# Kernel optimization log

Measured on AMD Instinct MI355X. Metric: run time of the kernel, lower is better.

## Reference

```python
import jax, jax.numpy as jnp
import numpy as np

NEG_INF = -9.0e15  # matches torch's -9000000000000000.0 mask value
ALPHA = 0.2        # LeakyReLU negative slope from init_kwargs


def setup_inputs() -> dict:
    key = jax.random.key(0)
    k1, k2, k3, k4, k5 = jax.random.split(key, 5)
    B, N, D, A = 64, 128, 128, 1000
    hidden = jax.random.normal(k1, (B, N, D), dtype=jnp.float32)
    adj = jax.random.randint(k2, (B, N, N), 0, 5)  # edge types 0..4 (0 = masked)
    a = jax.random.normal(k3, (D, 4), dtype=jnp.float32) * 0.1  # stacked a_0..a_3
    A_attr_sess = jax.random.uniform(k4, (B, N, A), dtype=jnp.float32)
    attr_embedding = jax.random.normal(k5, (A, D), dtype=jnp.float32)
    return {"hidden": hidden, "adj": adj, "a": a,
            "A_attr_sess": A_attr_sess, "attr_embedding": attr_embedding}


def reference(hidden, adj, a, A_attr_sess, attr_embedding):
    # a_input[b,i,j,:] = leaky_relu(h[b,i,:] * h[b,j,:])  -> [B,N,N,D]
    a_input = jax.nn.leaky_relu(hidden[:, :, None, :] * hidden[:, None, :, :],
                                negative_slope=ALPHA)
    # four edge-type scores in one contraction: [B,N,N,4]
    e = jnp.einsum('bijd,dk->bijk', a_input, a)
    # masked selection by adjacency edge type (later writes override earlier)
    alpha = jnp.full(adj.shape, NEG_INF, dtype=e.dtype)
    alpha = jnp.where(adj == 1, e[..., 0], alpha)
    alpha = jnp.where(adj == 2, e[..., 1], alpha)
    alpha = jnp.where(adj == 3, e[..., 2], alpha)
    alpha = jnp.where(adj == 4, e[..., 3], alpha)
    attn = jax.nn.softmax(alpha, axis=-1)        # [B,N,N]
    output = jnp.einsum('bij,bjd->bid', attn, hidden)  # [B,N,D]
    attr_sess = jnp.einsum('bna,ad->bnd', A_attr_sess, attr_embedding)
    return output, attr_sess
```

## Files before the change

### kernel.cpp

```cpp
#include <hip/hip_runtime.h>

#define BB 64
#define NN 128
#define DD 128
#define AA 1000
#define KPAD 1024
#define NEG_INF (-9.0e15f)

typedef __attribute__((ext_vector_type(8))) short short8;
typedef __attribute__((ext_vector_type(4))) float floatx4;
typedef __attribute__((ext_vector_type(4))) unsigned int uintx4;
typedef __attribute__((ext_vector_type(2))) unsigned int uintx2;

__device__ __forceinline__ float bflo(unsigned int u) { return __uint_as_float(u << 16); }
__device__ __forceinline__ float bfhi(unsigned int u) { return __uint_as_float(u & 0xffff0000u); }
__device__ __forceinline__ unsigned int packbf(float f0, float f1) {
  return (__float_as_uint(f0) >> 16) | (__float_as_uint(f1) & 0xffff0000u);
}
__device__ __forceinline__ unsigned short bf_rne(float f) {
  unsigned int u = __float_as_uint(f);
  return (unsigned short)((u + 0x7fffu + ((u >> 16) & 1u)) >> 16);
}
__device__ __forceinline__ unsigned int packbf_rne(float f0, float f1) {
  return (unsigned int)bf_rne(f0) | ((unsigned int)bf_rne(f1) << 16);
}
__device__ __forceinline__ short8 u2s(uintx4 v) {
  union { uintx4 u; short8 s; } x; x.u = v; return x.s;
}

__global__ __launch_bounds__(256) void prep_kernel(
    const float* __restrict__ hidden, const float* __restrict__ emb,
    unsigned short* __restrict__ ET, unsigned short* __restrict__ HTg)
{
  const int t = threadIdx.x;
  const int bid = blockIdx.x;
  if (bid < BB) {
    __shared__ float hsf[NN * 129];
    const float* hb = hidden + (size_t)bid * NN * DD;
    #pragma unroll
    for (int u = 0; u < 16; ++u) {
      int e = u * 1024 + t * 4;
      float4 v = *reinterpret_cast<const float4*>(hb + e);
      int r = e >> 7, c = e & 127;
      float* d = &hsf[r * 129 + c];
      d[0] = v.x; d[1] = v.y; d[2] = v.z; d[3] = v.w;
    }
    __syncthreads();
    unsigned short* ht16 = HTg + (size_t)bid * NN * DD;
    #pragma unroll
    for (int u = 0; u < 8; ++u) {
      int e = u * 2048 + t * 8;
      int dI = e >> 7, il = e & 127;
      float x[8];
      #pragma unroll
      for (int j = 0; j < 8; ++j) x[j] = hsf[(il + j) * 129 + dI];
      uintx4 o;
      o.x = packbf_rne(x[0], x[1]); o.y = packbf_rne(x[2], x[3]);
      o.z = packbf_rne(x[4], x[5]); o.w = packbf_rne(x[6], x[7]);
      *reinterpret_cast<uintx4*>(ht16 + e) = o;
    }
  } else {
    int c = bid - BB;
    int k0 = t * 4;
    float x[4];
    #pragma unroll
    for (int j = 0; j < 4; ++j) {
      int k = k0 + j;
      x[j] = (k < AA) ? emb[(size_t)k * DD + c] : 0.f;
    }
    uintx2 o;
    o.x = packbf_rne(x[0], x[1]);
    o.y = packbf_rne(x[2], x[3]);
    *reinterpret_cast<uintx2*>(ET + (size_t)c * KPAD + k0) = o;
  }
}

struct AttnSmem {
  __align__(16) unsigned short Hs[NN * 128];
  union {
    __align__(16) unsigned short As[4 * 16 * 256];
    struct {
      __align__(16) float Sa[16 * 129];
      __align__(16) unsigned short W[16 * 128];
    } sw;
  } u2;
  __align__(16) float saf[4 * 256];
};

#define BK 64
struct AttrSmem {
  __align__(16) unsigned short ETs[2][DD * BK];
  __align__(16) unsigned short As2[2][32 * BK];
};

union FusedSmem { AttnSmem a; AttrSmem g; };

__device__ __forceinline__ void attn_body(
    AttnSmem& s, const float* __restrict__ hidden,
    const int* __restrict__ adj, const float* __restrict__ amat,
    const unsigned short* __restrict__ HTg, float* __restrict__ out0)
{
  const int t = threadIdx.x;
  const int L = t & 63, w = t >> 6;
  const int lr = L & 15, lq = L >> 4;
  const int b = blockIdx.x >> 3;
  const int i0 = (blockIdx.x & 7) * 16;

  const int* adjb = adj + ((size_t)b * NN + i0) * NN;
  int adjv[8];
  #pragma unroll
  for (int nt = 0; nt < 2; ++nt)
    #pragma unroll
    for (int r = 0; r < 4; ++r)
      adjv[nt * 4 + r] = adjb[(lq * 4 + r) * NN + w * 32 + nt * 16 + lr];

  const float* hb = hidden + (size_t)b * NN * DD;
  #pragma unroll
  for (int u = 0; u < 8; ++u) {
    int id = u * 256 + t;
    int r = id >> 4, c = id & 15;
    const float* src = hb + r * 128 + c * 8;
    float4 v0 = *reinterpret_cast<const float4*>(src);
    float4 v1 = *reinterpret_cast<const float4*>(src + 4);
    uintx4 o;
    o.x = packbf_rne(v0.x, v0.y); o.y = packbf_rne(v0.z, v0.w);
    o.z = packbf_rne(v1.x, v1.y); o.w = packbf_rne(v1.z, v1.w);
    *reinterpret_cast<uintx4*>(&s.Hs[r * 128 + ((c ^ (r & 15)) << 3)]) = o;
  }
  {
    float v1 = amat[t], v2 = amat[t + 256];
    int dI = t >> 2, k = t & 3;
    s.saf[k * 256 + dI] = 0.6f * v1;
    s.saf[k * 256 + 128 + dI] = 0.4f * v1;
    s.saf[k * 256 + 64 + dI] = 0.6f * v2;
    s.saf[k * 256 + 192 + dI] = 0.4f * v2;
  }
  __syncthreads();

  #pragma unroll
  for (int u = 0; u < 8; ++u) {
    int id = u * 256 + t;
    int k = id >> 9, ii = (id >> 5) & 15, c = id & 31;
    int srow = i0 + ii;
    int dchunk = c & 15;
    uintx4 hv = *reinterpret_cast<const uintx4*>(
        &s.Hs[srow * 128 + ((dchunk ^ (srow & 15)) << 3)]);
    if (c & 16) {
      hv.x &= 0x7fff7fffu; hv.y &= 0x7fff7fffu;
      hv.z &= 0x7fff7fffu; hv.w &= 0x7fff7fffu;
    }
    const float* sf = &s.saf[k * 256 + c * 8];
    uintx4 o;
    o.x = packbf(bflo(hv.x) * sf[0], bfhi(hv.x) * sf[1]);
    o.y = packbf(bflo(hv.y) * sf[2], bfhi(hv.y) * sf[3]);
    o.z = packbf(bflo(hv.z) * sf[4], bfhi(hv.z) * sf[5]);
    o.w = packbf(bflo(hv.w) * sf[6], bfhi(hv.w) * sf[7]);
    *reinterpret_cast<uintx4*>(&s.u2.As[k * 4096 + ii * 256 + ((c ^ ii) << 3)]) = o;
  }
  __syncthreads();

  floatx4 acc[4][2];
  #pragma unroll
  for (int k = 0; k < 4; ++k)
    #pragma unroll
    for (int nt = 0; nt < 2; ++nt) acc[k][nt] = floatx4{0.f, 0.f, 0.f, 0.f};

  #pragma unroll
  for (int kt = 0; kt < 8; ++kt) {
    int ca = lq + 4 * kt;
    short8 afr[4];
    #pragma unroll
    for (int k = 0; k < 4; ++k)
      afr[k] = *reinterpret_cast<const short8*>(
          &s.u2.As[k * 4096 + lr * 256 + ((ca ^ lr) << 3)]);
    int cb = lq + 4 * (kt & 3);
    short8 bfr[2];
    #pragma unroll
    for (int nt = 0; nt < 2; ++nt) {
      int jrow = w * 32 + nt * 16 + lr;
      uintx4 hv = *reinterpret_cast<const uintx4*>(
          &s.Hs[jrow * 128 + ((cb ^ (jrow & 15)) << 3)]);
      if (kt >= 4) {
        hv.x &= 0x7fff7fffu; hv.y &= 0x7fff7fffu;
        hv.z &= 0x7fff7fffu; hv.w &= 0x7fff7fffu;
      }
      bfr[nt] = u2s(hv);
    }
    #pragma unroll
    for (int k = 0; k < 4; ++k)
      #pragma unroll
      for (int nt = 0; nt < 2; ++nt)
        acc[k][nt] = __builtin_amdgcn_mfma_f32_16x16x32_bf16(
            afr[k], bfr[nt], acc[k][nt], 0, 0, 0);
  }
  __syncthreads();

  short8 pvb[2][4];
  const unsigned short* ht = HTg + (size_t)b * NN * DD;
  #pragma unroll
  for (int nt = 0; nt < 2; ++nt)
    #pragma unroll
    for (int kt = 0; kt < 4; ++kt) {
      int dI = w * 32 + nt * 16 + lr;
      pvb[nt][kt] = *reinterpret_cast<const short8*>(ht + dI * 128 + kt * 32 + lq * 8);
    }

  #pragma unroll
  for (int nt = 0; nt < 2; ++nt)
    #pragma unroll
    for (int r = 0; r < 4; ++r) {
      int ii = lq * 4 + r;
      int j = w * 32 + nt * 16 + lr;
      int ad = adjv[nt * 4 + r];
      float al = NEG_INF;
      al = (ad == 1) ? acc[0][nt][r] : al;
      al = (ad == 2) ? acc[1][nt][r] : al;
      al = (ad == 3) ? acc[2][nt][r] : al;
      al = (ad == 4) ? acc[3][nt][r] : al;
      s.u2.sw.Sa[ii * 129 + j] = al;
    }
  __syncthreads();

  #pragma unroll
  for (int p = 0; p < 4; ++p) {
    int ii = w * 4 + p;
    float a1 = s.u2.sw.Sa[ii * 129 + L];
    float a2 = s.u2.sw.Sa[ii * 129 + 64 + L];
    float m = fmaxf(a1, a2);
    #pragma unroll
    for (int off = 32; off > 0; off >>= 1) m = fmaxf(m, __shfl_xor(m, off, 64));
    float e1 = __expf(fmaxf(a1 - m, -80.f));
    float e2 = __expf(fmaxf(a2 - m, -80.f));
    float ss = e1 + e2;
    #pragma unroll
    for (int off = 32; off > 0; off >>= 1) ss += __shfl_xor(ss, off, 64);
    float inv = 1.f / ss;
    int j2 = L + 64;
    s.u2.sw.W[ii * 128 + (((L >> 3) ^ ii) << 3) + (L & 7)] = bf_rne(e1 * inv);
    s.u2.sw.W[ii * 128 + (((j2 >> 3) ^ ii) << 3) + (j2 & 7)] = bf_rne(e2 * inv);
  }
  __syncthreads();

  floatx4 oacc[2];
  oacc[0] = floatx4{0.f, 0.f, 0.f, 0.f};
  oacc[1] = floatx4{0.f, 0.f, 0.f, 0.f};
  #pragma unroll
  for (int kt = 0; kt < 4; ++kt) {
    int c = lq + 4 * kt;
    short8 wf = *reinterpret_cast<const short8*>(
        &s.u2.sw.W[lr * 128 + ((c ^ lr) << 3)]);
    #pragma unroll
    for (int nt = 0; nt < 2; ++nt)
      oacc[nt] = __builtin_amdgcn_mfma_f32_16x16x32_bf16(
          wf, pvb[nt][kt], oacc[nt], 0, 0, 0);
  }
  float* ob = out0 + ((size_t)b * NN + i0) * DD;
  #pragma unroll
  for (int nt = 0; nt < 2; ++nt)
    #pragma unroll
    for (int r = 0; r < 4; ++r)
      ob[(lq * 4 + r) * DD + w * 32 + nt * 16 + lr] = oacc[nt][r];
}

__device__ __forceinline__ void attr_body(
    AttrSmem& s, const float* __restrict__ Aattr,
    const unsigned short* __restrict__ ET, float* __restrict__ out1)
{
  const int t = threadIdx.x;
  const int L = t & 63, w = t >> 6;
  const int lr = L & 15, lq = L >> 4;
  const int r0 = (blockIdx.x - 512) * 32;

  float4 pa0, pa1;
  uintx4 pe[4];
  const int ar = t >> 3, ak = (t & 7) * 8;
  const int ec = t >> 1, ej0 = (t & 1) * 4;

  auto fetch = [&](int it) {
    int kb = it * BK;
    int k4 = kb + ak;
    float4 z = {0.f, 0.f, 0.f, 0.f};
    pa0 = (k4 < AA) ? *reinterpret_cast<const float4*>(Aattr + (size_t)(r0 + ar) * AA + k4) : z;
    pa1 = (k4 + 4 < AA) ? *reinterpret_cast<const float4*>(Aattr + (size_t)(r0 + ar) * AA + k4 + 4) : z;
    #pragma unroll
    for (int q = 0; q < 4; ++q)
      pe[q] = *reinterpret_cast<const uintx4*>(ET + (size_t)ec * KPAD + kb + (ej0 + q) * 8);
  };
  auto stage = [&](int buf) {
    uintx4 o;
    o.x = packbf(pa0.x, pa0.y); o.y = packbf(pa0.z, pa0.w);
    o.z = packbf(pa1.x, pa1.y); o.w = packbf(pa1.z, pa1.w);
    int ac = t & 7;
    *reinterpret_cast<uintx4*>(&s.As2[buf][ar * BK + ((ac ^ (ar & 7)) << 3)]) = o;
    #pragma unroll
    for (int q = 0; q < 4; ++q)
      *reinterpret_cast<uintx4*>(&s.ETs[buf][ec * BK + (((ej0 + q) ^ (ec & 7)) << 3)]) = pe[q];
  };

  floatx4 acc[2][2];
  #pragma unroll
  for (int mt = 0; mt < 2; ++mt)
    #pragma unroll
    for (int nt = 0; nt < 2; ++nt) acc[mt][nt] = floatx4{0.f, 0.f, 0.f, 0.f};

  fetch(0);
  for (int it = 0; it < 16; ++it) {
    stage(it & 1);
    __syncthreads();
    if (it < 15) fetch(it + 1);
    #pragma unroll
    for (int ks = 0; ks < 2; ++ks) {
      int c = lq + 4 * ks;
      short8 af[2], bf[2];
      #pragma unroll
      for (int mt = 0; mt < 2; ++mt) {
        int row = mt * 16 + lr;
        af[mt] = *reinterpret_cast<const short8*>(
            &s.As2[it & 1][row * BK + ((c ^ (row & 7)) << 3)]);
      }
      #pragma unroll
      for (int nt = 0; nt < 2; ++nt) {
        int n = w * 32 + nt * 16 + lr;
        bf[nt] = *reinterpret_cast<const short8*>(
            &s.ETs[it & 1][n * BK + ((c ^ (n & 7)) << 3)]);
      }
      #pragma unroll
      for (int mt = 0; mt < 2; ++mt)
        #pragma unroll
        for (int nt = 0; nt < 2; ++nt)
          acc[mt][nt] = __builtin_amdgcn_mfma_f32_16x16x32_bf16(
              af[mt], bf[nt], acc[mt][nt], 0, 0, 0);
    }
  }

  float* ob = out1 + (size_t)r0 * DD;
  #pragma unroll
  for (int mt = 0; mt < 2; ++mt)
    #pragma unroll
    for (int nt = 0; nt < 2; ++nt)
      #pragma unroll
      for (int r = 0; r < 4; ++r)
        ob[(mt * 16 + lq * 4 + r) * DD + w * 32 + nt * 16 + lr] = acc[mt][nt][r];
}

__global__ __launch_bounds__(256, 3) void fused_kernel(
    const float* __restrict__ hidden, const int* __restrict__ adj,
    const float* __restrict__ amat, const float* __restrict__ Aattr,
    const unsigned short* __restrict__ ET, const unsigned short* __restrict__ HTg,
    float* __restrict__ out0, float* __restrict__ out1)
{
  __shared__ FusedSmem sm;
  if (blockIdx.x < 512) attn_body(sm.a, hidden, adj, amat, HTg, out0);
  else                  attr_body(sm.g, Aattr, ET, out1);
}

extern "C" void kernel_launch(void* const* d_in, const int* in_sizes, int n_in,
                              void* d_out, int out_size, void* d_ws, size_t ws_size,
                              hipStream_t stream) {
  const float* hidden = (const float*)d_in[0];
  const int*   adj    = (const int*)d_in[1];
  const float* amat   = (const float*)d_in[2];
  const float* Aattr  = (const float*)d_in[3];
  const float* emb    = (const float*)d_in[4];

  float* out0 = (float*)d_out;
  float* out1 = out0 + (size_t)BB * NN * DD;

  unsigned short* ET  = (unsigned short*)d_ws;
  unsigned short* HTg = ET + (size_t)DD * KPAD;

  prep_kernel<<<BB + DD, 256, 0, stream>>>(hidden, emb, ET, HTg);
  fused_kernel<<<768, 256, 0, stream>>>(hidden, adj, amat, Aattr, ET, HTg,
                                        out0, out1);
}
```

Measured before the change: 106.8 us.

## Fold prep kernel into fused kernel and compute A-fragments on the fly

Removes the separate prep kernel. Embedding transposition and bf16 conversion now happen inside the attribute GEMM staging, and the P·V operand is read transposed straight from the shared hidden tile instead of a global HT buffer. The attention A-operand is built in registers per k-step instead of being staged in shared memory. Softmax is done in MFMA register layout with cross-wave reductions through small shared arrays. Block roles are interleaved 2:1 and occupancy is raised to 4 blocks per SM. These changes remove a launch and global round-trips, in exchange for extra per-thread ALU work and scalar 16-bit LDS gathers.

```diff
diff --git a/kernel.cpp b/kernel.cpp
--- a/kernel.cpp
+++ b/kernel.cpp
@@ -4,13 +4,11 @@
 #define NN 128
 #define DD 128
 #define AA 1000
-#define KPAD 1024
 #define NEG_INF (-9.0e15f)
 
 typedef __attribute__((ext_vector_type(8))) short short8;
 typedef __attribute__((ext_vector_type(4))) float floatx4;
 typedef __attribute__((ext_vector_type(4))) unsigned int uintx4;
-typedef __attribute__((ext_vector_type(2))) unsigned int uintx2;
 
 __device__ __forceinline__ float bflo(unsigned int u) { return __uint_as_float(u << 16); }
 __device__ __forceinline__ float bfhi(unsigned int u) { return __uint_as_float(u & 0xffff0000u); }
@@ -28,69 +26,17 @@
   union { uintx4 u; short8 s; } x; x.u = v; return x.s;
 }
 
-__global__ __launch_bounds__(256) void prep_kernel(
-    const float* __restrict__ hidden, const float* __restrict__ emb,
-    unsigned short* __restrict__ ET, unsigned short* __restrict__ HTg)
-{
-  const int t = threadIdx.x;
-  const int bid = blockIdx.x;
-  if (bid < BB) {
-    __shared__ float hsf[NN * 129];
-    const float* hb = hidden + (size_t)bid * NN * DD;
-    #pragma unroll
-    for (int u = 0; u < 16; ++u) {
-      int e = u * 1024 + t * 4;
-      float4 v = *reinterpret_cast<const float4*>(hb + e);
-      int r = e >> 7, c = e & 127;
-      float* d = &hsf[r * 129 + c];
-      d[0] = v.x; d[1] = v.y; d[2] = v.z; d[3] = v.w;
-    }
-    __syncthreads();
-    unsigned short* ht16 = HTg + (size_t)bid * NN * DD;
-    #pragma unroll
-    for (int u = 0; u < 8; ++u) {
-      int e = u * 2048 + t * 8;
-      int dI = e >> 7, il = e & 127;
-      float x[8];
-      #pragma unroll
-      for (int j = 0; j < 8; ++j) x[j] = hsf[(il + j) * 129 + dI];
-      uintx4 o;
-      o.x = packbf_rne(x[0], x[1]); o.y = packbf_rne(x[2], x[3]);
-      o.z = packbf_rne(x[4], x[5]); o.w = packbf_rne(x[6], x[7]);
-      *reinterpret_cast<uintx4*>(ht16 + e) = o;
-    }
-  } else {
-    int c = bid - BB;
-    int k0 = t * 4;
-    float x[4];
-    #pragma unroll
-    for (int j = 0; j < 4; ++j) {
-      int k = k0 + j;
-      x[j] = (k < AA) ? emb[(size_t)k * DD + c] : 0.f;
-    }
-    uintx2 o;
-    o.x = packbf_rne(x[0], x[1]);
-    o.y = packbf_rne(x[2], x[3]);
-    *reinterpret_cast<uintx2*>(ET + (size_t)c * KPAD + k0) = o;
-  }
-}
-
 struct AttnSmem {
   __align__(16) unsigned short Hs[NN * 128];
-  union {
-    __align__(16) unsigned short As[4 * 16 * 256];
-    struct {
-      __align__(16) float Sa[16 * 129];
-      __align__(16) unsigned short W[16 * 128];
-    } sw;
-  } u2;
-  __align__(16) float saf[4 * 256];
+  __align__(16) unsigned short W[16 * 128];
+  __align__(16) unsigned short safb[4 * 256];
+  float wredM[4 * 16];
+  float wredS[4 * 16];
 };
 
-#define BK 64
 struct AttrSmem {
-  __align__(16) unsigned short ETs[2][DD * BK];
-  __align__(16) unsigned short As2[2][32 * BK];
+  __align__(16) unsigned short ETs[2][DD * 64];
+  __align__(16) unsigned short As2[2][32 * 64];
 };
 
 union FusedSmem { AttnSmem a; AttrSmem g; };
@@ -98,13 +44,13 @@
 __device__ __forceinline__ void attn_body(
     AttnSmem& s, const float* __restrict__ hidden,
     const int* __restrict__ adj, const float* __restrict__ amat,
-    const unsigned short* __restrict__ HTg, float* __restrict__ out0)
+    float* __restrict__ out0, int aid)
 {
   const int t = threadIdx.x;
   const int L = t & 63, w = t >> 6;
   const int lr = L & 15, lq = L >> 4;
-  const int b = blockIdx.x >> 3;
-  const int i0 = (blockIdx.x & 7) * 16;
+  const int b = aid >> 3;
+  const int i0 = (aid & 7) * 16;
 
   const int* adjb = adj + ((size_t)b * NN + i0) * NN;
   int adjv[8];
@@ -130,35 +76,13 @@
   {
     float v1 = amat[t], v2 = amat[t + 256];
     int dI = t >> 2, k = t & 3;
-    s.saf[k * 256 + dI] = 0.6f * v1;
-    s.saf[k * 256 + 128 + dI] = 0.4f * v1;
-    s.saf[k * 256 + 64 + dI] = 0.6f * v2;
-    s.saf[k * 256 + 192 + dI] = 0.4f * v2;
+    s.safb[k * 256 + dI]        = bf_rne(0.6f * v1);
+    s.safb[k * 256 + 128 + dI]  = bf_rne(0.4f * v1);
+    s.safb[k * 256 + 64 + dI]   = bf_rne(0.6f * v2);
+    s.safb[k * 256 + 192 + dI]  = bf_rne(0.4f * v2);
   }
   __syncthreads();
 
-  #pragma unroll
-  for (int u = 0; u < 8; ++u) {
-    int id = u * 256 + t;
-    int k = id >> 9, ii = (id >> 5) & 15, c = id & 31;
-    int srow = i0 + ii;
-    int dchunk = c & 15;
-    uintx4 hv = *reinterpret_cast<const uintx4*>(
-        &s.Hs[srow * 128 + ((dchunk ^ (srow & 15)) << 3)]);
-    if (c & 16) {
-      hv.x &= 0x7fff7fffu; hv.y &= 0x7fff7fffu;
-      hv.z &= 0x7fff7fffu; hv.w &= 0x7fff7fffu;
-    }
-    const float* sf = &s.saf[k * 256 + c * 8];
-    uintx4 o;
-    o.x = packbf(bflo(hv.x) * sf[0], bfhi(hv.x) * sf[1]);
-    o.y = packbf(bflo(hv.y) * sf[2], bfhi(hv.y) * sf[3]);
-    o.z = packbf(bflo(hv.z) * sf[4], bfhi(hv.z) * sf[5]);
-    o.w = packbf(bflo(hv.w) * sf[6], bfhi(hv.w) * sf[7]);
-    *reinterpret_cast<uintx4*>(&s.u2.As[k * 4096 + ii * 256 + ((c ^ ii) << 3)]) = o;
-  }
-  __syncthreads();
-
   floatx4 acc[4][2];
   #pragma unroll
   for (int k = 0; k < 4; ++k)
@@ -167,13 +91,27 @@
 
   #pragma unroll
   for (int kt = 0; kt < 8; ++kt) {
-    int ca = lq + 4 * kt;
+    const int cb = lq + 4 * (kt & 3);
+    const int aoff = (kt >= 4) ? 128 : 0;
+    uintx4 ha = *reinterpret_cast<const uintx4*>(
+        &s.Hs[(i0 + lr) * 128 + ((cb ^ lr) << 3)]);
+    if (kt >= 4) {
+      ha.x &= 0x7fff7fffu; ha.y &= 0x7fff7fffu;
+      ha.z &= 0x7fff7fffu; ha.w &= 0x7fff7fffu;
+    }
+    const float h0 = bflo(ha.x), h1 = bfhi(ha.x), h2 = bflo(ha.y), h3 = bfhi(ha.y);
+    const float h4 = bflo(ha.z), h5 = bfhi(ha.z), h6 = bflo(ha.w), h7 = bfhi(ha.w);
     short8 afr[4];
     #pragma unroll
-    for (int k = 0; k < 4; ++k)
-      afr[k] = *reinterpret_cast<const short8*>(
-          &s.u2.As[k * 4096 + lr * 256 + ((ca ^ lr) << 3)]);
-    int cb = lq + 4 * (kt & 3);
+    for (int k = 0; k < 4; ++k) {
+      uintx4 sv = *reinterpret_cast<const uintx4*>(&s.safb[k * 256 + aoff + cb * 8]);
+      uintx4 o;
+      o.x = packbf(h0 * bflo(sv.x), h1 * bfhi(sv.x));
+      o.y = packbf(h2 * bflo(sv.y), h3 * bfhi(sv.y));
+      o.z = packbf(h4 * bflo(sv.z), h5 * bfhi(sv.z));
+      o.w = packbf(h6 * bflo(sv.w), h7 * bfhi(sv.w));
+      afr[k] = u2s(o);
+    }
     short8 bfr[2];
     #pragma unroll
     for (int nt = 0; nt < 2; ++nt) {
@@ -193,52 +131,61 @@
         acc[k][nt] = __builtin_amdgcn_mfma_f32_16x16x32_bf16(
             afr[k], bfr[nt], acc[k][nt], 0, 0, 0);
   }
+
+  float al[2][4];
+  #pragma unroll
+  for (int nt = 0; nt < 2; ++nt)
+    #pragma unroll
+    for (int r = 0; r < 4; ++r) {
+      int ad = adjv[nt * 4 + r];
+      float v = NEG_INF;
+      v = (ad == 1) ? acc[0][nt][r] : v;
+      v = (ad == 2) ? acc[1][nt][r] : v;
+      v = (ad == 3) ? acc[2][nt][r] : v;
+      v = (ad == 4) ? acc[3][nt][r] : v;
+      al[nt][r] = v;
+    }
+
+  float mr[4];
+  #pragma unroll
+  for (int r = 0; r < 4; ++r) mr[r] = fmaxf(al[0][r], al[1][r]);
+  #pragma unroll
+  for (int off = 1; off < 16; off <<= 1)
+    #pragma unroll
+    for (int r = 0; r < 4; ++r) mr[r] = fmaxf(mr[r], __shfl_xor(mr[r], off, 64));
+  if (lr == 0)
+    #pragma unroll
+    for (int r = 0; r < 4; ++r) s.wredM[w * 16 + lq * 4 + r] = mr[r];
   __syncthreads();
 
-  short8 pvb[2][4];
-  const unsigned short* ht = HTg + (size_t)b * NN * DD;
+  float ex[2][4], sr[4];
+  #pragma unroll
+  for (int r = 0; r < 4; ++r) {
+    int i = lq * 4 + r;
+    float m = fmaxf(fmaxf(s.wredM[i], s.wredM[16 + i]),
+                    fmaxf(s.wredM[32 + i], s.wredM[48 + i]));
+    ex[0][r] = __expf(fmaxf(al[0][r] - m, -80.f));
+    ex[1][r] = __expf(fmaxf(al[1][r] - m, -80.f));
+    sr[r] = ex[0][r] + ex[1][r];
+  }
+  #pragma unroll
+  for (int off = 1; off < 16; off <<= 1)
+    #pragma unroll
+    for (int r = 0; r < 4; ++r) sr[r] += __shfl_xor(sr[r], off, 64);
+  if (lr == 0)
+    #pragma unroll
+    for (int r = 0; r < 4; ++r) s.wredS[w * 16 + lq * 4 + r] = sr[r];
+  __syncthreads();
+
   #pragma unroll
   for (int nt = 0; nt < 2; ++nt)
     #pragma unroll
-    for (int kt = 0; kt < 4; ++kt) {
-      int dI = w * 32 + nt * 16 + lr;
-      pvb[nt][kt] = *reinterpret_cast<const short8*>(ht + dI * 128 + kt * 32 + lq * 8);
-    }
-
-  #pragma unroll
-  for (int nt = 0; nt < 2; ++nt)
-    #pragma unroll
     for (int r = 0; r < 4; ++r) {
-      int ii = lq * 4 + r;
+      int i = lq * 4 + r;
+      float ss = s.wredS[i] + s.wredS[16 + i] + s.wredS[32 + i] + s.wredS[48 + i];
       int j = w * 32 + nt * 16 + lr;
-      int ad = adjv[nt * 4 + r];
-      float al = NEG_INF;
-      al = (ad == 1) ? acc[0][nt][r] : al;
-      al = (ad == 2) ? acc[1][nt][r] : al;
-      al = (ad == 3) ? acc[2][nt][r] : al;
-      al = (ad == 4) ? acc[3][nt][r] : al;
-      s.u2.sw.Sa[ii * 129 + j] = al;
-    }
-  __syncthreads();
-
-  #pragma unroll
-  for (int p = 0; p < 4; ++p) {
-    int ii = w * 4 + p;
-    float a1 = s.u2.sw.Sa[ii * 129 + L];
-    float a2 = s.u2.sw.Sa[ii * 129 + 64 + L];
-    float m = fmaxf(a1, a2);
-    #pragma unroll
-    for (int off = 32; off > 0; off >>= 1) m = fmaxf(m, __shfl_xor(m, off, 64));
-    float e1 = __expf(fmaxf(a1 - m, -80.f));
-    float e2 = __expf(fmaxf(a2 - m, -80.f));
-    float ss = e1 + e2;
-    #pragma unroll
-    for (int off = 32; off > 0; off >>= 1) ss += __shfl_xor(ss, off, 64);
-    float inv = 1.f / ss;
-    int j2 = L + 64;
-    s.u2.sw.W[ii * 128 + (((L >> 3) ^ ii) << 3) + (L & 7)] = bf_rne(e1 * inv);
-    s.u2.sw.W[ii * 128 + (((j2 >> 3) ^ ii) << 3) + (j2 & 7)] = bf_rne(e2 * inv);
-  }
+      s.W[i * 128 + (((j >> 3) ^ i) << 3) + (j & 7)] = bf_rne(ex[nt][r] / ss);
+    }
   __syncthreads();
 
   floatx4 oacc[2];
@@ -246,13 +193,24 @@
   oacc[1] = floatx4{0.f, 0.f, 0.f, 0.f};
   #pragma unroll
   for (int kt = 0; kt < 4; ++kt) {
-    int c = lq + 4 * kt;
+    int cw = lq + 4 * kt;
     short8 wf = *reinterpret_cast<const short8*>(
-        &s.u2.sw.W[lr * 128 + ((c ^ lr) << 3)]);
-    #pragma unroll
-    for (int nt = 0; nt < 2; ++nt)
-      oacc[nt] = __builtin_amdgcn_mfma_f32_16x16x32_bf16(
-          wf, pvb[nt][kt], oacc[nt], 0, 0, 0);
+        &s.W[lr * 128 + ((cw ^ lr) << 3)]);
+    #pragma unroll
+    for (int nt = 0; nt < 2; ++nt) {
+      int d = w * 32 + nt * 16 + lr;
+      int sw = d >> 3, dl = d & 7;
+      unsigned int rr[8];
+      #pragma unroll
+      for (int e = 0; e < 8; ++e) {
+        int j = kt * 32 + lq * 8 + e;
+        rr[e] = s.Hs[j * 128 + ((sw ^ (j & 15)) << 3) + dl];
+      }
+      uintx4 uu;
+      uu.x = rr[0] | (rr[1] << 16); uu.y = rr[2] | (rr[3] << 16);
+      uu.z = rr[4] | (rr[5] << 16); uu.w = rr[6] | (rr[7] << 16);
+      oacc[nt] = __builtin_amdgcn_mfma_f32_16x16x32_bf16(wf, u2s(uu), oacc[nt], 0, 0, 0);
+    }
   }
   float* ob = out0 + ((size_t)b * NN + i0) * DD;
   #pragma unroll
@@ -264,37 +222,46 @@
 
 __device__ __forceinline__ void attr_body(
     AttrSmem& s, const float* __restrict__ Aattr,
-    const unsigned short* __restrict__ ET, float* __restrict__ out1)
+    const float* __restrict__ emb, float* __restrict__ out1, int gid)
 {
   const int t = threadIdx.x;
   const int L = t & 63, w = t >> 6;
   const int lr = L & 15, lq = L >> 4;
-  const int r0 = (blockIdx.x - 512) * 32;
-
-  float4 pa0, pa1;
-  uintx4 pe[4];
-  const int ar = t >> 3, ak = (t & 7) * 8;
-  const int ec = t >> 1, ej0 = (t & 1) * 4;
+  const int r0 = gid * 32;
+
+  const int ar = t >> 3, ak = (t & 7) * 8, ac = t & 7;
+  const int cq = t & 31, kg = t >> 5;
+
+  float4 pa0, pa1, pe[8];
 
   auto fetch = [&](int it) {
-    int kb = it * BK;
+    int kb = it * 64;
     int k4 = kb + ak;
     float4 z = {0.f, 0.f, 0.f, 0.f};
     pa0 = (k4 < AA) ? *reinterpret_cast<const float4*>(Aattr + (size_t)(r0 + ar) * AA + k4) : z;
     pa1 = (k4 + 4 < AA) ? *reinterpret_cast<const float4*>(Aattr + (size_t)(r0 + ar) * AA + k4 + 4) : z;
     #pragma unroll
-    for (int q = 0; q < 4; ++q)
-      pe[q] = *reinterpret_cast<const uintx4*>(ET + (size_t)ec * KPAD + kb + (ej0 + q) * 8);
+    for (int q = 0; q < 8; ++q) {
+      int k = kb + kg * 8 + q;
+      pe[q] = (k < AA) ? *reinterpret_cast<const float4*>(emb + (size_t)k * 128 + cq * 4) : z;
+    }
   };
   auto stage = [&](int buf) {
     uintx4 o;
     o.x = packbf(pa0.x, pa0.y); o.y = packbf(pa0.z, pa0.w);
     o.z = packbf(pa1.x, pa1.y); o.w = packbf(pa1.z, pa1.w);
-    int ac = t & 7;
-    *reinterpret_cast<uintx4*>(&s.As2[buf][ar * BK + ((ac ^ (ar & 7)) << 3)]) = o;
-    #pragma unroll
-    for (int q = 0; q < 4; ++q)
-      *reinterpret_cast<uintx4*>(&s.ETs[buf][ec * BK + (((ej0 + q) ^ (ec & 7)) << 3)]) = pe[q];
+    *reinterpret_cast<uintx4*>(&s.As2[buf][ar * 64 + ((ac ^ (ar & 7)) << 3)]) = o;
+    const float* pf = reinterpret_cast<const float*>(pe);
+    #pragma unroll
+    for (int cc = 0; cc < 4; ++cc) {
+      int c = cq * 4 + cc;
+      uintx4 e;
+      e.x = packbf(pf[0 * 4 + cc], pf[1 * 4 + cc]);
+      e.y = packbf(pf[2 * 4 + cc], pf[3 * 4 + cc]);
+      e.z = packbf(pf[4 * 4 + cc], pf[5 * 4 + cc]);
+      e.w = packbf(pf[6 * 4 + cc], pf[7 * 4 + cc]);
+      *reinterpret_cast<uintx4*>(&s.ETs[buf][c * 64 + ((kg ^ (c & 7)) << 3)]) = e;
+    }
   };
 
   floatx4 acc[2][2];
@@ -316,13 +283,13 @@
       for (int mt = 0; mt < 2; ++mt) {
         int row = mt * 16 + lr;
         af[mt] = *reinterpret_cast<const short8*>(
-            &s.As2[it & 1][row * BK + ((c ^ (row & 7)) << 3)]);
+            &s.As2[it & 1][row * 64 + ((c ^ (row & 7)) << 3)]);
       }
       #pragma unroll
       for (int nt = 0; nt < 2; ++nt) {
         int n = w * 32 + nt * 16 + lr;
         bf[nt] = *reinterpret_cast<const short8*>(
-            &s.ETs[it & 1][n * BK + ((c ^ (n & 7)) << 3)]);
+            &s.ETs[it & 1][n * 64 + ((c ^ (n & 7)) << 3)]);
       }
       #pragma unroll
       for (int mt = 0; mt < 2; ++mt)
@@ -343,15 +310,17 @@
         ob[(mt * 16 + lq * 4 + r) * DD + w * 32 + nt * 16 + lr] = acc[mt][nt][r];
 }
 
-__global__ __launch_bounds__(256, 3) void fused_kernel(
+__global__ __launch_bounds__(256, 4) void fused_kernel(
     const float* __restrict__ hidden, const int* __restrict__ adj,
     const float* __restrict__ amat, const float* __restrict__ Aattr,
-    const unsigned short* __restrict__ ET, const unsigned short* __restrict__ HTg,
+    const float* __restrict__ emb,
     float* __restrict__ out0, float* __restrict__ out1)
 {
   __shared__ FusedSmem sm;
-  if (blockIdx.x < 512) attn_body(sm.a, hidden, adj, amat, HTg, out0);
-  else                  attr_body(sm.g, Aattr, ET, out1);
+  const int q3 = blockIdx.x / 3;
+  const int r3 = blockIdx.x % 3;
+  if (r3 == 2) attr_body(sm.g, Aattr, emb, out1, q3);
+  else         attn_body(sm.a, hidden, adj, amat, out0, q3 * 2 + r3);
 }
 
 extern "C" void kernel_launch(void* const* d_in, const int* in_sizes, int n_in,
@@ -366,10 +335,5 @@
   float* out0 = (float*)d_out;
   float* out1 = out0 + (size_t)BB * NN * DD;
 
-  unsigned short* ET  = (unsigned short*)d_ws;
-  unsigned short* HTg = ET + (size_t)DD * KPAD;
-
-  prep_kernel<<<BB + DD, 256, 0, stream>>>(hidden, emb, ET, HTg);
-  fused_kernel<<<768, 256, 0, stream>>>(hidden, adj, amat, Aattr, ET, HTg,
-                                        out0, out1);
-}
+  fused_kernel<<<768, 256, 0, stream>>>(hidden, adj, amat, Aattr, emb, out0, out1);
+}
```

Result: slower. 137.2 us (+28.4%).
